# Optimization experiments

Measured on AMD Instinct MI355X. Metric: run time of the kernel, lower is better.

Reference implementation:

```python
import jax, jax.numpy as jnp
import numpy as np

B, T, D_IN, H, N_CLASSES = 32, 64, 10000, 200, 2


def setup_inputs() -> dict:
    key = jax.random.key(0)
    ks = jax.random.split(key, 16)
    s_in = 1.0 / np.sqrt(H)  # torch nn.RNN init scale
    def u(k, shape):
        return jax.random.uniform(k, shape, jnp.float32, -s_in, s_in)
    inp = {"x": jax.random.normal(ks[0], (B, T, D_IN), jnp.float32)}
    dims = [D_IN, H, H]
    for l in range(3):
        inp[f"W_ih{l}"] = u(ks[1 + 4 * l], (H, dims[l]))
        inp[f"W_hh{l}"] = u(ks[2 + 4 * l], (H, H))
        inp[f"b_ih{l}"] = u(ks[3 + 4 * l], (H,))
        inp[f"b_hh{l}"] = u(ks[4 + 4 * l], (H,))
    inp["fc_w"] = u(ks[13], (N_CLASSES, H))
    inp["fc_b"] = u(ks[14], (N_CLASSES,))
    return inp


def _rnn_layer(x_seq, W_ih, W_hh, b_ih, b_hh):
    # x_seq: [B, T, D] -> hidden sequence [B, T, H]
    pre = jnp.einsum('btd,hd->bth', x_seq, W_ih) + b_ih + b_hh  # input proj batched over time
    h0 = jnp.zeros((x_seq.shape[0], W_hh.shape[0]), x_seq.dtype)

    def step(h, p_t):
        h_new = jnp.tanh(p_t + h @ W_hh.T)
        return h_new, h_new

    _, hs = jax.lax.scan(step, h0, jnp.swapaxes(pre, 0, 1))  # [T, B, H]
    return jnp.swapaxes(hs, 0, 1)


def reference(x, W_ih0, W_hh0, b_ih0, b_hh0, W_ih1, W_hh1, b_ih1, b_hh1,
              W_ih2, W_hh2, b_ih2, b_hh2, fc_w, fc_b):
    h = _rnn_layer(x, W_ih0, W_hh0, b_ih0, b_hh0)
    h = _rnn_layer(h, W_ih1, W_hh1, b_ih1, b_hh1)
    h = _rnn_layer(h, W_ih2, W_hh2, b_ih2, b_hh2)
    last = h[:, -1, :]  # [B, H]; dropout is identity at inference
    logits = last @ fc_w.T + fc_b  # [B, n_classes]
    return logits
```

## Files before the change

### kernel.cpp

```cpp
#include <hip/hip_runtime.h>
#include <hip/hip_bf16.h>


typedef __bf16  bf16x8 __attribute__((ext_vector_type(8)));
typedef float   f32x4  __attribute__((ext_vector_type(4)));

#define HDIM 200
#define BM 128
#define CHUNK_B 26624
#define MFMA(a, b, c) __builtin_amdgcn_mfma_f32_16x16x32_bf16(a, b, c, 0, 0, 0)

__device__ __forceinline__ void glds16(const void* g, void* l) {
    __builtin_amdgcn_global_load_lds(
        (const __attribute__((address_space(1))) unsigned int*)g,
        (__attribute__((address_space(3))) unsigned int*)l, 16, 0, 0);
}

__global__ void pack_w(const float* __restrict__ W, int K, int nkc,
                       __bf16* __restrict__ out)
{
    const int total = nkc * 1664;
    for (int g = blockIdx.x * blockDim.x + threadIdx.x; g < total;
         g += gridDim.x * blockDim.x) {
        const int kc = g / 1664;
        const int o  = g - kc * 1664;
        const int isLo = (o >= 832);
        const int o2 = isLo ? o - 832 : o;
        const int r  = o2 >> 2;
        const int k  = kc * 32 + (o2 & 3) * 8;
        bf16x8 v;
        if (r < HDIM && k < K) {
            const float* p = W + (size_t)r * K + k;
            float4 a = *(const float4*)p, b = *(const float4*)(p + 4);
            float f[8] = {a.x, a.y, a.z, a.w, b.x, b.y, b.z, b.w};
#pragma unroll
            for (int i = 0; i < 8; ++i) {
                __bf16 h = (__bf16)f[i];
                v[i] = isLo ? (__bf16)(f[i] - (float)h) : h;
            }
        } else {
#pragma unroll
            for (int i = 0; i < 8; ++i) v[i] = (__bf16)0.f;
        }
        *(bf16x8*)&out[(size_t)g * 8] = v;
    }
}

__global__ __launch_bounds__(512, 1)
void gemm_pipe(const float* __restrict__ A, int lda, int K,
               const __bf16* __restrict__ Bpack,
               float* __restrict__ Cbase, int per_split, int ksteps)
{
    __shared__ alignas(16) __bf16 Ab[2][8192];
    __shared__ alignas(16) __bf16 Bb[2][13312];

    const int tid = threadIdx.x;
    const int kc0 = blockIdx.y * ksteps;
    const int m0  = blockIdx.x * BM;
    float* __restrict__ C = Cbase + (size_t)blockIdx.y * per_split;

    const int wv = tid >> 6, lane = tid & 63;
    const int r16 = lane & 15, kg = lane >> 4;
    const int mg = wv & 3, ng = wv >> 2;
    const int nt0 = ng * 7, ntw = ng ? 6 : 7;

    const int a_row = tid >> 2;
    const int a_q   = tid & 3;
    const float* Arow = A + (size_t)(m0 + a_row) * lda + a_q * 8;

    f32x4 acc[2][7];
#pragma unroll
    for (int mi = 0; mi < 2; ++mi)
#pragma unroll
        for (int j = 0; j < 7; ++j) acc[mi][j] = (f32x4)0.f;

    float av[8];
    auto loadA = [&](int ks) {
        const int kb = (kc0 + ks) * 32;
        if (kb + a_q * 8 < K) {
            const float* p = Arow + kb;
            float4 x0 = *(const float4*)p, x1 = *(const float4*)(p + 4);
            av[0]=x0.x; av[1]=x0.y; av[2]=x0.z; av[3]=x0.w;
            av[4]=x1.x; av[5]=x1.y; av[6]=x1.z; av[7]=x1.w;
        } else {
#pragma unroll
            for (int i = 0; i < 8; ++i) av[i] = 0.f;
        }
    };
    auto issueB = [&](int ks, int buf) {
        const char* src = (const char*)Bpack + (size_t)(kc0 + ks) * CHUNK_B;
        char* dst = (char*)&Bb[buf][0];
#pragma unroll
        for (int r = 0; r < 3; ++r)
            glds16(src + (r * 512 + tid) * 16, dst + (r * 512 + tid) * 16);
        if (tid < 128)
            glds16(src + (1536 + tid) * 16, dst + (1536 + tid) * 16);
    };

    loadA(0);
    issueB(0, 0);

    for (int ks = 0; ks < ksteps; ++ks) {
        const int cur = ks & 1, nxt = cur ^ 1;
        bf16x8 th, tl;
#pragma unroll
        for (int i = 0; i < 8; ++i) {
            __bf16 h = (__bf16)av[i];
            th[i] = h; tl[i] = (__bf16)(av[i] - (float)h);
        }
        *(bf16x8*)&Ab[cur][a_row * 32 + a_q * 8]        = th;
        *(bf16x8*)&Ab[cur][4096 + a_row * 32 + a_q * 8] = tl;
        __syncthreads();
        if (ks + 1 < ksteps) { issueB(ks + 1, nxt); loadA(ks + 1); }

        const int ao0 = (mg * 32 + r16) * 32 + kg * 8;
        const int ao1 = ao0 + 16 * 32;
        bf16x8 ah0 = *(const bf16x8*)&Ab[cur][ao0];
        bf16x8 al0 = *(const bf16x8*)&Ab[cur][4096 + ao0];
        bf16x8 ah1 = *(const bf16x8*)&Ab[cur][ao1];
        bf16x8 al1 = *(const bf16x8*)&Ab[cur][4096 + ao1];
#pragma unroll
        for (int j = 0; j < 7; ++j) {
            if (j < ntw) {
                const int bo = ((nt0 + j) * 16 + r16) * 32 + kg * 8;
                bf16x8 bh = *(const bf16x8*)&Bb[cur][bo];
                bf16x8 bl = *(const bf16x8*)&Bb[cur][6656 + bo];
                acc[0][j] = MFMA(al0, bh, acc[0][j]);
                acc[0][j] = MFMA(ah0, bl, acc[0][j]);
                acc[0][j] = MFMA(ah0, bh, acc[0][j]);
                acc[1][j] = MFMA(al1, bh, acc[1][j]);
                acc[1][j] = MFMA(ah1, bl, acc[1][j]);
                acc[1][j] = MFMA(ah1, bh, acc[1][j]);
            }
        }
    }

#pragma unroll
    for (int mi = 0; mi < 2; ++mi) {
        const int rb = m0 + (mg * 2 + mi) * 16 + kg * 4;
#pragma unroll
        for (int j = 0; j < 7; ++j) {
            if (j < ntw) {
                const int n = (nt0 + j) * 16 + r16;
                if (n < HDIM)
#pragma unroll
                    for (int r = 0; r < 4; ++r)
                        C[(size_t)(rb + r) * HDIM + n] = acc[mi][j][r];
            }
        }
    }
}

__global__ void reduce_parts(const float* __restrict__ Pp, float* __restrict__ P)
{
    const int i = blockIdx.x * blockDim.x + threadIdx.x;
    if (i < 102400) {
        float4 s = ((const float4*)Pp)[i];
#pragma unroll
        for (int r = 1; r < 16; ++r) {
            float4 v = ((const float4*)Pp)[(size_t)r * 102400 + i];
            s.x += v.x; s.y += v.y; s.z += v.z; s.w += v.w;
        }
        ((float4*)P)[i] = s;
    }
}

__device__ __forceinline__ float fast_tanh(float x) {
    float e = __expf(-2.f * fabsf(x));
    float r = (1.f - e) / (1.f + e);
    return copysignf(r, x);
}

__global__ __launch_bounds__(512, 1)
void rnn_rec(const float* __restrict__ pre,
             const float* __restrict__ Whh,
             const float* __restrict__ bih,
             const float* __restrict__ bhh,
             float* __restrict__ Hout)
{
    const int b   = blockIdx.x;
    const int tid = threadIdx.x;

    __shared__ float preS[64 * HDIM];
    __shared__ float h[HDIM];
    __shared__ float bias[HDIM];
    __shared__ float part[10][HDIM];

    {
        const float4* ps = (const float4*)(pre + (size_t)b * 64 * HDIM);
        float4* pd = (float4*)preS;
        for (int i = tid; i < 3200; i += 512) pd[i] = ps[i];
    }

    const bool act = tid < 500;
    const int g  = tid / 10;
    const int s  = tid - g * 10;
    const int n0 = g * 4;
    const int k0 = s * 20;

    float w[80];
    if (act) {
#pragma unroll
        for (int j = 0; j < 4; ++j) {
            const float* wr = Whh + (size_t)(n0 + j) * HDIM + k0;
#pragma unroll
            for (int i = 0; i < 5; ++i) {
                float4 v = *(const float4*)(wr + i * 4);
                w[j * 20 + i * 4 + 0] = v.x; w[j * 20 + i * 4 + 1] = v.y;
                w[j * 20 + i * 4 + 2] = v.z; w[j * 20 + i * 4 + 3] = v.w;
            }
        }
    }
    if (tid < HDIM) { bias[tid] = bih[tid] + bhh[tid]; h[tid] = 0.f; }
    __syncthreads();

    for (int t = 0; t < 64; ++t) {
        if (act) {
            float a0 = 0.f, a1 = 0.f, a2 = 0.f, a3 = 0.f;
#pragma unroll
            for (int i = 0; i < 5; ++i) {
                float4 hv = *(const float4*)&h[k0 + i * 4];
                a0 += w[ 0 + i*4]*hv.x + w[ 1 + i*4]*hv.y + w[ 2 + i*4]*hv.z + w[ 3 + i*4]*hv.w;
                a1 += w[20 + i*4]*hv.x + w[21 + i*4]*hv.y + w[22 + i*4]*hv.z + w[23 + i*4]*hv.w;
                a2 += w[40 + i*4]*hv.x + w[41 + i*4]*hv.y + w[42 + i*4]*hv.z + w[43 + i*4]*hv.w;
                a3 += w[60 + i*4]*hv.x + w[61 + i*4]*hv.y + w[62 + i*4]*hv.z + w[63 + i*4]*hv.w;
            }
            float4 pv = make_float4(a0, a1, a2, a3);
            *(float4*)&part[s][n0] = pv;
        }
        __syncthreads();
        if (tid < HDIM) {
            float sum = part[0][tid];
#pragma unroll
            for (int r = 1; r < 10; ++r) sum += part[r][tid];
            float v = fast_tanh(sum + preS[t * HDIM + tid] + bias[tid]);
            h[tid] = v;
            Hout[((size_t)b * 64 + t) * HDIM + tid] = v;
        }
        __syncthreads();
    }
}


__global__ void fc_head(const float* __restrict__ Hlast_base,
                        const float* __restrict__ fcw,
                        const float* __restrict__ fcb,
                        float* __restrict__ out)
{
    const int i = threadIdx.x;
    if (i >= 64) return;
    const int b = i >> 1, cls = i & 1;
    const float* hp = Hlast_base + ((size_t)b * 64 + 63) * HDIM;
    const float* fw = fcw + cls * HDIM;
    float s = fcb[cls];
    for (int j = 0; j < HDIM; ++j) s += hp[j] * fw[j];
    out[b * 2 + cls] = s;
}

extern "C" void kernel_launch(void* const* d_in, const int* in_sizes, int n_in,
                              void* d_out, int out_size, void* d_ws, size_t ws_size,
                              hipStream_t stream) {
    const float* x     = (const float*)d_in[0];
    const float* W_ih0 = (const float*)d_in[1];
    const float* W_hh0 = (const float*)d_in[2];
    const float* b_ih0 = (const float*)d_in[3];
    const float* b_hh0 = (const float*)d_in[4];
    const float* W_ih1 = (const float*)d_in[5];
    const float* W_hh1 = (const float*)d_in[6];
    const float* b_ih1 = (const float*)d_in[7];
    const float* b_hh1 = (const float*)d_in[8];
    const float* W_ih2 = (const float*)d_in[9];
    const float* W_hh2 = (const float*)d_in[10];
    const float* b_ih2 = (const float*)d_in[11];
    const float* b_hh2 = (const float*)d_in[12];
    const float* fc_w  = (const float*)d_in[13];
    const float* fc_b  = (const float*)d_in[14];
    float* out = (float*)d_out;

    const size_t PE = (size_t)2048 * HDIM;
    float* P     = (float*)d_ws;
    float* Hbuf  = P + PE;
    float* Hbuf2 = Hbuf + PE;
    float* Ppart = Hbuf2 + PE;
    __bf16* W0p  = (__bf16*)(Ppart + 16 * PE);
    __bf16* W1p  = W0p + (size_t)320 * 13312;
    __bf16* W2p  = W1p + (size_t)7 * 13312;

    pack_w<<<1024, 256, 0, stream>>>(W_ih0, 10000, 320, W0p);
    pack_w<<<46, 256, 0, stream>>>(W_ih1, HDIM, 7, W1p);
    pack_w<<<46, 256, 0, stream>>>(W_ih2, HDIM, 7, W2p);

    gemm_pipe<<<dim3(16, 16), 512, 0, stream>>>(x, 10000, 10000, W0p, Ppart, (int)PE, 20);
    reduce_parts<<<400, 256, 0, stream>>>(Ppart, P);
    rnn_rec<<<32, 512, 0, stream>>>(P, W_hh0, b_ih0, b_hh0, Hbuf);

    gemm_pipe<<<dim3(16, 1), 512, 0, stream>>>(Hbuf, HDIM, HDIM, W1p, P, (int)PE, 7);
    rnn_rec<<<32, 512, 0, stream>>>(P, W_hh1, b_ih1, b_hh1, Hbuf2);

    gemm_pipe<<<dim3(16, 1), 512, 0, stream>>>(Hbuf2, HDIM, HDIM, W2p, P, (int)PE, 7);
    rnn_rec<<<32, 512, 0, stream>>>(P, W_hh2, b_ih2, b_hh2, Hbuf);

    fc_head<<<1, 64, 0, stream>>>(Hbuf, fc_w, fc_b, out);
}
```

Before: 332.7 us.

## Pad LDS rows, replace split-K reduce with atomics, shuffle-reduce RNN recurrence

Pads the bf16 tiles in LDS from a row stride of 32 to 40 elements to cut bank conflicts, and repacks the weights to match. The separate split-K reduction kernel and its 16 partial buffers are replaced by a memset followed by atomicAdd accumulation in the GEMM epilogue. The recurrent kernel now splits each output group over 8 lanes, reduces with xor shuffles, double-buffers h, and uses one raw barrier per timestep instead of two syncthreads plus a shared partial-sum pass. The atomics make the summation order nondeterministic.

```diff
diff --git a/kernel.cpp b/kernel.cpp
--- a/kernel.cpp
+++ b/kernel.cpp
@@ -7,7 +7,9 @@
 
 #define HDIM 200
 #define BM 128
-#define CHUNK_B 26624
+#define ROWP 40
+#define CHUNK_ELEMS (2 * 208 * ROWP)
+#define CHUNK_16B   (CHUNK_ELEMS / 8)
 #define MFMA(a, b, c) __builtin_amdgcn_mfma_f32_16x16x32_bf16(a, b, c, 0, 0, 0)
 
 __device__ __forceinline__ void glds16(const void* g, void* l) {
@@ -19,28 +21,23 @@
 __global__ void pack_w(const float* __restrict__ W, int K, int nkc,
                        __bf16* __restrict__ out)
 {
-    const int total = nkc * 1664;
+    const int total = nkc * CHUNK_16B;
     for (int g = blockIdx.x * blockDim.x + threadIdx.x; g < total;
          g += gridDim.x * blockDim.x) {
-        const int kc = g / 1664;
-        const int o  = g - kc * 1664;
-        const int isLo = (o >= 832);
-        const int o2 = isLo ? o - 832 : o;
-        const int r  = o2 >> 2;
-        const int k  = kc * 32 + (o2 & 3) * 8;
+        const int kc = g / CHUNK_16B;
+        const int o  = g - kc * CHUNK_16B;
+        const int isLo = (o >= 1040);
+        const int o2 = isLo ? o - 1040 : o;
+        const int r  = o2 / 5;
+        const int cq = (o2 - r * 5) * 8;
         bf16x8 v;
-        if (r < HDIM && k < K) {
-            const float* p = W + (size_t)r * K + k;
-            float4 a = *(const float4*)p, b = *(const float4*)(p + 4);
-            float f[8] = {a.x, a.y, a.z, a.w, b.x, b.y, b.z, b.w};
-#pragma unroll
-            for (int i = 0; i < 8; ++i) {
-                __bf16 h = (__bf16)f[i];
-                v[i] = isLo ? (__bf16)(f[i] - (float)h) : h;
-            }
-        } else {
-#pragma unroll
-            for (int i = 0; i < 8; ++i) v[i] = (__bf16)0.f;
+#pragma unroll
+        for (int i = 0; i < 8; ++i) {
+            const int c = cq + i;
+            const int k = kc * 32 + c;
+            float f = (r < HDIM && c < 32 && k < K) ? W[(size_t)r * K + k] : 0.f;
+            __bf16 h = (__bf16)f;
+            v[i] = isLo ? (__bf16)(f - (float)h) : h;
         }
         *(bf16x8*)&out[(size_t)g * 8] = v;
     }
@@ -49,15 +46,14 @@
 __global__ __launch_bounds__(512, 1)
 void gemm_pipe(const float* __restrict__ A, int lda, int K,
                const __bf16* __restrict__ Bpack,
-               float* __restrict__ Cbase, int per_split, int ksteps)
+               float* __restrict__ C, int ksteps, int accumulate)
 {
-    __shared__ alignas(16) __bf16 Ab[2][8192];
-    __shared__ alignas(16) __bf16 Bb[2][13312];
+    __shared__ alignas(16) __bf16 Ab[2][2 * 128 * ROWP];
+    __shared__ alignas(16) __bf16 Bb[2][CHUNK_ELEMS];
 
     const int tid = threadIdx.x;
     const int kc0 = blockIdx.y * ksteps;
     const int m0  = blockIdx.x * BM;
-    float* __restrict__ C = Cbase + (size_t)blockIdx.y * per_split;
 
     const int wv = tid >> 6, lane = tid & 63;
     const int r16 = lane & 15, kg = lane >> 4;
@@ -88,13 +84,13 @@
         }
     };
     auto issueB = [&](int ks, int buf) {
-        const char* src = (const char*)Bpack + (size_t)(kc0 + ks) * CHUNK_B;
+        const char* src = (const char*)Bpack + (size_t)(kc0 + ks) * (CHUNK_16B * 16);
         char* dst = (char*)&Bb[buf][0];
 #pragma unroll
-        for (int r = 0; r < 3; ++r)
+        for (int r = 0; r < 4; ++r)
             glds16(src + (r * 512 + tid) * 16, dst + (r * 512 + tid) * 16);
-        if (tid < 128)
-            glds16(src + (1536 + tid) * 16, dst + (1536 + tid) * 16);
+        if (tid < 32)
+            glds16(src + (2048 + tid) * 16, dst + (2048 + tid) * 16);
     };
 
     loadA(0);
@@ -108,23 +104,23 @@
             __bf16 h = (__bf16)av[i];
             th[i] = h; tl[i] = (__bf16)(av[i] - (float)h);
         }
-        *(bf16x8*)&Ab[cur][a_row * 32 + a_q * 8]        = th;
-        *(bf16x8*)&Ab[cur][4096 + a_row * 32 + a_q * 8] = tl;
+        *(bf16x8*)&Ab[cur][a_row * ROWP + a_q * 8]              = th;
+        *(bf16x8*)&Ab[cur][128 * ROWP + a_row * ROWP + a_q * 8] = tl;
         __syncthreads();
         if (ks + 1 < ksteps) { issueB(ks + 1, nxt); loadA(ks + 1); }
 
-        const int ao0 = (mg * 32 + r16) * 32 + kg * 8;
-        const int ao1 = ao0 + 16 * 32;
+        const int ao0 = (mg * 32 + r16) * ROWP + kg * 8;
+        const int ao1 = ao0 + 16 * ROWP;
         bf16x8 ah0 = *(const bf16x8*)&Ab[cur][ao0];
-        bf16x8 al0 = *(const bf16x8*)&Ab[cur][4096 + ao0];
+        bf16x8 al0 = *(const bf16x8*)&Ab[cur][128 * ROWP + ao0];
         bf16x8 ah1 = *(const bf16x8*)&Ab[cur][ao1];
-        bf16x8 al1 = *(const bf16x8*)&Ab[cur][4096 + ao1];
+        bf16x8 al1 = *(const bf16x8*)&Ab[cur][128 * ROWP + ao1];
 #pragma unroll
         for (int j = 0; j < 7; ++j) {
             if (j < ntw) {
-                const int bo = ((nt0 + j) * 16 + r16) * 32 + kg * 8;
+                const int bo = ((nt0 + j) * 16 + r16) * ROWP + kg * 8;
                 bf16x8 bh = *(const bf16x8*)&Bb[cur][bo];
-                bf16x8 bl = *(const bf16x8*)&Bb[cur][6656 + bo];
+                bf16x8 bl = *(const bf16x8*)&Bb[cur][208 * ROWP + bo];
                 acc[0][j] = MFMA(al0, bh, acc[0][j]);
                 acc[0][j] = MFMA(ah0, bl, acc[0][j]);
                 acc[0][j] = MFMA(ah0, bh, acc[0][j]);
@@ -142,26 +138,19 @@
         for (int j = 0; j < 7; ++j) {
             if (j < ntw) {
                 const int n = (nt0 + j) * 16 + r16;
-                if (n < HDIM)
-#pragma unroll
-                    for (int r = 0; r < 4; ++r)
-                        C[(size_t)(rb + r) * HDIM + n] = acc[mi][j][r];
-            }
-        }
-    }
-}
-
-__global__ void reduce_parts(const float* __restrict__ Pp, float* __restrict__ P)
-{
-    const int i = blockIdx.x * blockDim.x + threadIdx.x;
-    if (i < 102400) {
-        float4 s = ((const float4*)Pp)[i];
-#pragma unroll
-        for (int r = 1; r < 16; ++r) {
-            float4 v = ((const float4*)Pp)[(size_t)r * 102400 + i];
-            s.x += v.x; s.y += v.y; s.z += v.z; s.w += v.w;
-        }
-        ((float4*)P)[i] = s;
+                if (n < HDIM) {
+                    if (accumulate) {
+#pragma unroll
+                        for (int r = 0; r < 4; ++r)
+                            atomicAdd(&C[(size_t)(rb + r) * HDIM + n], acc[mi][j][r]);
+                    } else {
+#pragma unroll
+                        for (int r = 0; r < 4; ++r)
+                            C[(size_t)(rb + r) * HDIM + n] = acc[mi][j][r];
+                    }
+                }
+            }
+        }
     }
 }
 
@@ -169,6 +158,10 @@
     float e = __expf(-2.f * fabsf(x));
     float r = (1.f - e) / (1.f + e);
     return copysignf(r, x);
+}
+
+__device__ __forceinline__ void raw_barrier() {
+    asm volatile("s_waitcnt lgkmcnt(0)\n\ts_barrier" ::: "memory");
 }
 
 __global__ __launch_bounds__(512, 1)
@@ -182,9 +175,7 @@
     const int tid = threadIdx.x;
 
     __shared__ float preS[64 * HDIM];
-    __shared__ float h[HDIM];
-    __shared__ float bias[HDIM];
-    __shared__ float part[10][HDIM];
+    __shared__ float h[2][HDIM];
 
     {
         const float4* ps = (const float4*)(pre + (size_t)b * 64 * HDIM);
@@ -192,55 +183,66 @@
         for (int i = tid; i < 3200; i += 512) pd[i] = ps[i];
     }
 
-    const bool act = tid < 500;
-    const int g  = tid / 10;
-    const int s  = tid - g * 10;
+    const int g = tid >> 3;
+    const int s = tid & 7;
+    const bool act = (g < 50);
     const int n0 = g * 4;
-    const int k0 = s * 20;
-
-    float w[80];
+    const int lo = s & 3;
+    const int base = 25 * s - lo;
+
+    float w[4][28];
+    float bv[4];
     if (act) {
 #pragma unroll
-        for (int j = 0; j < 4; ++j) {
-            const float* wr = Whh + (size_t)(n0 + j) * HDIM + k0;
-#pragma unroll
-            for (int i = 0; i < 5; ++i) {
-                float4 v = *(const float4*)(wr + i * 4);
-                w[j * 20 + i * 4 + 0] = v.x; w[j * 20 + i * 4 + 1] = v.y;
-                w[j * 20 + i * 4 + 2] = v.z; w[j * 20 + i * 4 + 3] = v.w;
-            }
-        }
-    }
-    if (tid < HDIM) { bias[tid] = bih[tid] + bhh[tid]; h[tid] = 0.f; }
+        for (int jn = 0; jn < 4; ++jn) {
+            const float* wr = Whh + (size_t)(n0 + jn) * HDIM;
+#pragma unroll
+            for (int c4 = 0; c4 < 7; ++c4) {
+                float4 v = *(const float4*)(wr + base + c4 * 4);
+                const float vv[4] = {v.x, v.y, v.z, v.w};
+#pragma unroll
+                for (int e = 0; e < 4; ++e) {
+                    const int c = c4 * 4 + e;
+                    w[jn][c] = (c >= lo && c < lo + 25) ? vv[e] : 0.f;
+                }
+            }
+            if (s == 0) bv[jn] = bih[n0 + jn] + bhh[n0 + jn];
+        }
+    }
+    if (tid < HDIM) h[0][tid] = 0.f;
     __syncthreads();
 
     for (int t = 0; t < 64; ++t) {
+        const int cur = t & 1, nxt = cur ^ 1;
         if (act) {
             float a0 = 0.f, a1 = 0.f, a2 = 0.f, a3 = 0.f;
 #pragma unroll
-            for (int i = 0; i < 5; ++i) {
-                float4 hv = *(const float4*)&h[k0 + i * 4];
-                a0 += w[ 0 + i*4]*hv.x + w[ 1 + i*4]*hv.y + w[ 2 + i*4]*hv.z + w[ 3 + i*4]*hv.w;
-                a1 += w[20 + i*4]*hv.x + w[21 + i*4]*hv.y + w[22 + i*4]*hv.z + w[23 + i*4]*hv.w;
-                a2 += w[40 + i*4]*hv.x + w[41 + i*4]*hv.y + w[42 + i*4]*hv.z + w[43 + i*4]*hv.w;
-                a3 += w[60 + i*4]*hv.x + w[61 + i*4]*hv.y + w[62 + i*4]*hv.z + w[63 + i*4]*hv.w;
-            }
-            float4 pv = make_float4(a0, a1, a2, a3);
-            *(float4*)&part[s][n0] = pv;
-        }
-        __syncthreads();
-        if (tid < HDIM) {
-            float sum = part[0][tid];
-#pragma unroll
-            for (int r = 1; r < 10; ++r) sum += part[r][tid];
-            float v = fast_tanh(sum + preS[t * HDIM + tid] + bias[tid]);
-            h[tid] = v;
-            Hout[((size_t)b * 64 + t) * HDIM + tid] = v;
-        }
-        __syncthreads();
-    }
-}
-
+            for (int c4 = 0; c4 < 7; ++c4) {
+                float4 hv = *(const float4*)&h[cur][base + c4 * 4];
+                a0 += w[0][c4*4+0]*hv.x + w[0][c4*4+1]*hv.y + w[0][c4*4+2]*hv.z + w[0][c4*4+3]*hv.w;
+                a1 += w[1][c4*4+0]*hv.x + w[1][c4*4+1]*hv.y + w[1][c4*4+2]*hv.z + w[1][c4*4+3]*hv.w;
+                a2 += w[2][c4*4+0]*hv.x + w[2][c4*4+1]*hv.y + w[2][c4*4+2]*hv.z + w[2][c4*4+3]*hv.w;
+                a3 += w[3][c4*4+0]*hv.x + w[3][c4*4+1]*hv.y + w[3][c4*4+2]*hv.z + w[3][c4*4+3]*hv.w;
+            }
+#pragma unroll
+            for (int m = 1; m <= 4; m <<= 1) {
+                a0 += __shfl_xor(a0, m); a1 += __shfl_xor(a1, m);
+                a2 += __shfl_xor(a2, m); a3 += __shfl_xor(a3, m);
+            }
+            if (s == 0) {
+                float4 pv = *(const float4*)&preS[t * HDIM + n0];
+                float v0 = fast_tanh(a0 + pv.x + bv[0]);
+                float v1 = fast_tanh(a1 + pv.y + bv[1]);
+                float v2 = fast_tanh(a2 + pv.z + bv[2]);
+                float v3 = fast_tanh(a3 + pv.w + bv[3]);
+                *(float4*)&h[nxt][n0] = make_float4(v0, v1, v2, v3);
+                *(float4*)&Hout[((size_t)b * 64 + t) * HDIM + n0] =
+                    make_float4(v0, v1, v2, v3);
+            }
+        }
+        raw_barrier();
+    }
+}
 
 __global__ void fc_head(const float* __restrict__ Hlast_base,
                         const float* __restrict__ fcw,
@@ -281,23 +283,22 @@
     float* P     = (float*)d_ws;
     float* Hbuf  = P + PE;
     float* Hbuf2 = Hbuf + PE;
-    float* Ppart = Hbuf2 + PE;
-    __bf16* W0p  = (__bf16*)(Ppart + 16 * PE);
-    __bf16* W1p  = W0p + (size_t)320 * 13312;
-    __bf16* W2p  = W1p + (size_t)7 * 13312;
+    __bf16* W0p  = (__bf16*)(Hbuf2 + PE);
+    __bf16* W1p  = W0p + (size_t)320 * CHUNK_ELEMS;
+    __bf16* W2p  = W1p + (size_t)7 * CHUNK_ELEMS;
 
     pack_w<<<1024, 256, 0, stream>>>(W_ih0, 10000, 320, W0p);
     pack_w<<<46, 256, 0, stream>>>(W_ih1, HDIM, 7, W1p);
     pack_w<<<46, 256, 0, stream>>>(W_ih2, HDIM, 7, W2p);
 
-    gemm_pipe<<<dim3(16, 16), 512, 0, stream>>>(x, 10000, 10000, W0p, Ppart, (int)PE, 20);
-    reduce_parts<<<400, 256, 0, stream>>>(Ppart, P);
+    hipMemsetAsync(P, 0, PE * sizeof(float), stream);
+    gemm_pipe<<<dim3(16, 16), 512, 0, stream>>>(x, 10000, 10000, W0p, P, 20, 1);
     rnn_rec<<<32, 512, 0, stream>>>(P, W_hh0, b_ih0, b_hh0, Hbuf);
 
-    gemm_pipe<<<dim3(16, 1), 512, 0, stream>>>(Hbuf, HDIM, HDIM, W1p, P, (int)PE, 7);
+    gemm_pipe<<<dim3(16, 1), 512, 0, stream>>>(Hbuf, HDIM, HDIM, W1p, P, 7, 0);
     rnn_rec<<<32, 512, 0, stream>>>(P, W_hh1, b_ih1, b_hh1, Hbuf2);
 
-    gemm_pipe<<<dim3(16, 1), 512, 0, stream>>>(Hbuf2, HDIM, HDIM, W2p, P, (int)PE, 7);
+    gemm_pipe<<<dim3(16, 1), 512, 0, stream>>>(Hbuf2, HDIM, HDIM, W2p, P, 7, 0);
     rnn_rec<<<32, 512, 0, stream>>>(P, W_hh2, b_ih2, b_hh2, Hbuf);
 
     fc_head<<<1, 64, 0, stream>>>(Hbuf, fc_w, fc_b, out);
```

Measured after the change: 497.3 us. 1.49x slower.
